# Kernel tuning notes

Hardware: AMD Instinct MI355X
Metric: run time of the kernel (lower is better)

Reference implementation:

```python
import jax, jax.numpy as jnp
import numpy as np


def setup_inputs() -> dict:
    key = jax.random.key(0)
    k1, k2, k3 = jax.random.split(key, 3)
    N, M, D = 8192, 32768, 64
    source_data = jax.random.normal(k1, (N, D), dtype=jnp.float32)
    target_data = jax.random.normal(k2, (M, D), dtype=jnp.float32)
    psi = jax.random.normal(k3, (M,), dtype=jnp.float32)
    return {"source_data": source_data, "target_data": target_data, "psi": psi}


def reference(source_data, target_data, psi):
    # cost[n, m] = ||x_n||^2 + ||y_m||^2 - 2 <x_n, y_m>
    sq_src = jnp.sum(source_data ** 2, axis=1, keepdims=True)          # [N, 1]
    sq_tgt = jnp.sum(target_data ** 2, axis=1)[None, :]                # [1, M]
    cost = sq_src + sq_tgt - 2.0 * jnp.einsum('nd,md->nm', source_data, target_data)
    out = jnp.min(cost - psi[None, :], axis=1) + jnp.mean(psi)         # [N]
    return out
```

## Files before the change

kernel.cpp:

```cpp
#include <hip/hip_runtime.h>
#include <stdint.h>

typedef float  f32x4v __attribute__((ext_vector_type(4)));
typedef short  s16x8  __attribute__((ext_vector_type(8)));

constexpr int D      = 64;
constexpr int SPLITS = 128;
constexpr int CHM    = 256;
constexpr int G      = 4;
constexpr int NT     = CHM / 16;

__device__ __forceinline__ unsigned short f2bf(float f) {
    unsigned int u = __float_as_uint(f);
    u = (u + 0x7FFFu + ((u >> 16) & 1u)) >> 16;
    return (unsigned short)u;
}

__device__ __forceinline__ void gload_lds16(const void* g, void* l) {
    __builtin_amdgcn_global_load_lds((__attribute__((address_space(1))) void*)g,
                                     (__attribute__((address_space(3))) void*)l, 16, 0, 0);
}
__device__ __forceinline__ void gload_lds4(const void* g, void* l) {
    __builtin_amdgcn_global_load_lds((__attribute__((address_space(1))) void*)g,
                                     (__attribute__((address_space(3))) void*)l, 4, 0, 0);
}

__global__ __launch_bounds__(256)
void prep(const float* __restrict__ X, const float* __restrict__ Y,
          const float* __restrict__ psi,
          unsigned short* __restrict__ Xb, unsigned short* __restrict__ Yb,
          float* __restrict__ t, float* __restrict__ sqx,
          float* __restrict__ psum_arr, int N, int M) {
    const int tid  = threadIdx.x;
    const int lane = tid & 63, wave = tid >> 6;
    const int r16  = lane & 15, q = lane >> 4;
    const int NYB = M >> 4, NXB = N >> 4;
    const int b = blockIdx.x;
    __shared__ float red[4];

    if (b < NYB) {
        const int row = b * 16 + wave * 4 + q;
        const float4 v = *reinterpret_cast<const float4*>(Y + (size_t)row * D + r16 * 4);
        uint2 p;
        p.x = (unsigned)f2bf(v.x) | ((unsigned)f2bf(v.y) << 16);
        p.y = (unsigned)f2bf(v.z) | ((unsigned)f2bf(v.w) << 16);
        *reinterpret_cast<uint2*>(Yb + (size_t)row * D + r16 * 4) = p;
        float s = v.x * v.x + v.y * v.y + v.z * v.z + v.w * v.w;
        #pragma unroll
        for (int off = 1; off <= 8; off <<= 1) s += __shfl_xor(s, off);
        if (r16 == 0) t[row] = s - psi[row];
    } else if (b < NYB + NXB) {
        const int row = (b - NYB) * 16 + wave * 4 + q;
        const float4 v = *reinterpret_cast<const float4*>(X + (size_t)row * D + r16 * 4);
        uint2 p;
        p.x = (unsigned)f2bf(-2.f * v.x) | ((unsigned)f2bf(-2.f * v.y) << 16);
        p.y = (unsigned)f2bf(-2.f * v.z) | ((unsigned)f2bf(-2.f * v.w) << 16);
        *reinterpret_cast<uint2*>(Xb + (size_t)row * D + r16 * 4) = p;
        float s = v.x * v.x + v.y * v.y + v.z * v.z + v.w * v.w;
        #pragma unroll
        for (int off = 1; off <= 8; off <<= 1) s += __shfl_xor(s, off);
        if (r16 == 0) sqx[row] = s;
    } else {
        const int g = b - NYB - NXB;
        float s = psi[g * 512 + tid] + psi[g * 512 + 256 + tid];
        #pragma unroll
        for (int off = 1; off <= 32; off <<= 1) s += __shfl_xor(s, off);
        if (lane == 0) red[wave] = s;
        __syncthreads();
        if (tid == 0) psum_arr[g] = red[0] + red[1] + red[2] + red[3];
    }
}

__global__ __launch_bounds__(256, 4)
void sdot_main(const unsigned short* __restrict__ Xb,
               const unsigned short* __restrict__ Yb,
               const float* __restrict__ t,
               float* __restrict__ partial, int M) {
    __shared__ __align__(16) unsigned short ly[CHM * D];
    __shared__ __align__(16) float lt[CHM];

    const int tid  = threadIdx.x;
    const int wave = tid >> 6, lane = tid & 63;
    const int quad = lane >> 4, r16 = lane & 15;
    const int chunk   = blockIdx.x;
    const int rowgrp  = blockIdx.y;
    const int m_begin = chunk * CHM;

    #pragma unroll
    for (int i = 0; i < 8; ++i) {
        const int idx = i * 256 + tid;
        const int row = idx >> 3, c = idx & 7;
        gload_lds16(Yb + (size_t)(m_begin + row) * D + ((c ^ (row & 7)) << 3),
                    &ly[(i * 256 + wave * 64) << 3]);
    }
    gload_lds4(t + m_begin + wave * 64 + lane, &lt[wave * 64]);

    s16x8 b[G][2];
    #pragma unroll
    for (int g = 0; g < G; ++g) {
        const int srow = rowgrp * 256 + wave * (G * 16) + g * 16 + r16;
        #pragma unroll
        for (int h = 0; h < 2; ++h)
            b[g][h] = *reinterpret_cast<const s16x8*>(Xb + (size_t)srow * D + h * 32 + quad * 8);
    }

    float rmin[G];
    #pragma unroll
    for (int g = 0; g < G; ++g) rmin[g] = 1e30f;

    asm volatile("s_waitcnt vmcnt(0)" ::: "memory");
    __builtin_amdgcn_s_barrier();

    const int csw0 = (quad ^ (r16 & 7)) << 3;
    const int csw1 = ((quad + 4) ^ (r16 & 7)) << 3;

#define SDOT_STEP(st, A_)                                                           \
    {                                                                               \
        const int trow = (st) * 16 + r16;                                           \
        const s16x8 a0 = *reinterpret_cast<const s16x8*>(&ly[trow * D + csw0]);     \
        const s16x8 a1 = *reinterpret_cast<const s16x8*>(&ly[trow * D + csw1]);     \
        const f32x4v tv4 = *reinterpret_cast<const f32x4v*>(&lt[(st) * 16 + quad * 4]); \
        __builtin_amdgcn_s_setprio(1);                                              \
        _Pragma("unroll")                                                           \
        for (int g = 0; g < G; ++g)                                                 \
            A_[g] = __builtin_amdgcn_mfma_f32_16x16x32_bf16(a0, b[g][0], tv4, 0, 0, 0); \
        _Pragma("unroll")                                                           \
        for (int g = 0; g < G; ++g)                                                 \
            A_[g] = __builtin_amdgcn_mfma_f32_16x16x32_bf16(a1, b[g][1], A_[g], 0, 0, 0); \
        __builtin_amdgcn_s_setprio(0);                                              \
    }
#define SDOT_FOLD(A_)                                                               \
    {                                                                               \
        _Pragma("unroll")                                                           \
        for (int g = 0; g < G; ++g)                                                 \
            rmin[g] = fminf(fminf(fminf(A_[g][0], A_[g][1]),                        \
                                  fminf(A_[g][2], A_[g][3])), rmin[g]);             \
    }

    f32x4v accA[G], accB[G];
    SDOT_STEP(0, accB);
    for (int p = 0; p < NT / 2 - 1; ++p) {
        SDOT_STEP(2 * p + 1, accA);  SDOT_FOLD(accB);
        SDOT_STEP(2 * p + 2, accB);  SDOT_FOLD(accA);
    }
    SDOT_STEP(NT - 1, accA);  SDOT_FOLD(accB);  SDOT_FOLD(accA);
#undef SDOT_STEP
#undef SDOT_FOLD

    #pragma unroll
    for (int off = 16; off <= 32; off <<= 1)
        #pragma unroll
        for (int g = 0; g < G; ++g)
            rmin[g] = fminf(rmin[g], __shfl_xor(rmin[g], off));

    if (quad == 0) {
        #pragma unroll
        for (int g = 0; g < G; ++g) {
            const int row = rowgrp * 256 + wave * (G * 16) + g * 16 + r16;
            partial[(size_t)row * SPLITS + chunk] = rmin[g];
        }
    }
}

__global__ __launch_bounds__(256)
void finalize(const float* __restrict__ sqx, const float* __restrict__ partial,
              const float* __restrict__ psum_arr, float* __restrict__ out, int M) {
    const int lane = threadIdx.x & 63, wave = threadIdx.x >> 6;
    const int row  = blockIdx.x * 4 + wave;
    float ps = psum_arr[lane];
    #pragma unroll
    for (int off = 1; off <= 32; off <<= 1) ps += __shfl_xor(ps, off);
    float pm = fminf(partial[(size_t)row * SPLITS + lane],
                     partial[(size_t)row * SPLITS + 64 + lane]);
    #pragma unroll
    for (int off = 1; off <= 32; off <<= 1) pm = fminf(pm, __shfl_xor(pm, off));
    if (lane == 0) out[row] = sqx[row] + ps / (float)M + pm;
}

extern "C" void kernel_launch(void* const* d_in, const int* in_sizes, int n_in,
                              void* d_out, int out_size, void* d_ws, size_t ws_size,
                              hipStream_t stream) {
    const float* X   = (const float*)d_in[0];
    const float* Y   = (const float*)d_in[1];
    const float* psi = (const float*)d_in[2];
    float* out = (float*)d_out;

    const int N = in_sizes[0] / D;
    const int M = in_sizes[2];

    char* ws = (char*)d_ws;
    unsigned short* Yb = (unsigned short*)ws;
    size_t off = (size_t)M * D * sizeof(unsigned short);
    unsigned short* Xb = (unsigned short*)(ws + off);
    off += (size_t)N * D * sizeof(unsigned short);
    float* t = (float*)(ws + off);
    off += (size_t)M * sizeof(float);
    float* sqx = (float*)(ws + off);
    off += (size_t)N * sizeof(float);
    float* partial = (float*)(ws + off);
    off += (size_t)N * SPLITS * sizeof(float);
    float* psum_arr = (float*)(ws + off);

    prep<<<(M >> 4) + (N >> 4) + 64, 256, 0, stream>>>(X, Y, psi, Xb, Yb, t, sqx, psum_arr, N, M);
    sdot_main<<<dim3(SPLITS, N / 256), 256, 0, stream>>>(Xb, Yb, t, partial, M);
    finalize<<<N / 4, 256, 0, stream>>>(sqx, partial, psum_arr, out, M);
}
```

Measured before the change: 103.9 us.

## Loop over double-buffered Y tiles per block with fewer M splits

```diff
diff --git a/kernel.cpp b/kernel.cpp
--- a/kernel.cpp
+++ b/kernel.cpp
@@ -5,10 +5,9 @@
 typedef short  s16x8  __attribute__((ext_vector_type(8)));
 
 constexpr int D      = 64;
-constexpr int SPLITS = 128;
-constexpr int CHM    = 256;
+constexpr int SPLITS = 32;
+constexpr int TILE_M = 128;
 constexpr int G      = 4;
-constexpr int NT     = CHM / 16;
 
 __device__ __forceinline__ unsigned short f2bf(float f) {
     unsigned int u = __float_as_uint(f);
@@ -76,24 +75,17 @@
                const unsigned short* __restrict__ Yb,
                const float* __restrict__ t,
                float* __restrict__ partial, int M) {
-    __shared__ __align__(16) unsigned short ly[CHM * D];
-    __shared__ __align__(16) float lt[CHM];
+    __shared__ __align__(16) unsigned short ly[2][TILE_M * 64];
+    __shared__ __align__(16) float lt[2][256];
 
     const int tid  = threadIdx.x;
     const int wave = tid >> 6, lane = tid & 63;
     const int quad = lane >> 4, r16 = lane & 15;
-    const int chunk   = blockIdx.x;
-    const int rowgrp  = blockIdx.y;
-    const int m_begin = chunk * CHM;
-
-    #pragma unroll
-    for (int i = 0; i < 8; ++i) {
-        const int idx = i * 256 + tid;
-        const int row = idx >> 3, c = idx & 7;
-        gload_lds16(Yb + (size_t)(m_begin + row) * D + ((c ^ (row & 7)) << 3),
-                    &ly[(i * 256 + wave * 64) << 3]);
-    }
-    gload_lds4(t + m_begin + wave * 64 + lane, &lt[wave * 64]);
+    const int chunk  = blockIdx.x;
+    const int rowgrp = blockIdx.y;
+    const int CH      = M / SPLITS;
+    const int m_begin = chunk * CH;
+    const int NTT     = CH / TILE_M;
 
     s16x8 b[G][2];
     #pragma unroll
@@ -108,6 +100,18 @@
     #pragma unroll
     for (int g = 0; g < G; ++g) rmin[g] = 1e30f;
 
+    auto stage = [&](int buf, int mb) {
+        #pragma unroll
+        for (int i = 0; i < 4; ++i) {
+            const int idx = i * 256 + tid;
+            const int row = idx >> 3, c = idx & 7;
+            gload_lds16(Yb + (size_t)(mb + row) * D + ((c ^ (row & 7)) << 3),
+                        &ly[buf][(i * 256 + wave * 64) << 3]);
+        }
+        gload_lds4(t + mb + wave * 64 + lane, &lt[buf][wave * 64]);
+    };
+
+    stage(0, m_begin);
     asm volatile("s_waitcnt vmcnt(0)" ::: "memory");
     __builtin_amdgcn_s_barrier();
 
@@ -117,9 +121,9 @@
 #define SDOT_STEP(st, A_)                                                           \
     {                                                                               \
         const int trow = (st) * 16 + r16;                                           \
-        const s16x8 a0 = *reinterpret_cast<const s16x8*>(&ly[trow * D + csw0]);     \
-        const s16x8 a1 = *reinterpret_cast<const s16x8*>(&ly[trow * D + csw1]);     \
-        const f32x4v tv4 = *reinterpret_cast<const f32x4v*>(&lt[(st) * 16 + quad * 4]); \
+        const s16x8 a0 = *reinterpret_cast<const s16x8*>(&ly[buf][trow * 64 + csw0]); \
+        const s16x8 a1 = *reinterpret_cast<const s16x8*>(&ly[buf][trow * 64 + csw1]); \
+        const f32x4v tv4 = *reinterpret_cast<const f32x4v*>(&lt[buf][(st) * 16 + quad * 4]); \
         __builtin_amdgcn_s_setprio(1);                                              \
         _Pragma("unroll")                                                           \
         for (int g = 0; g < G; ++g)                                                 \
@@ -138,12 +142,21 @@
     }
 
     f32x4v accA[G], accB[G];
-    SDOT_STEP(0, accB);
-    for (int p = 0; p < NT / 2 - 1; ++p) {
-        SDOT_STEP(2 * p + 1, accA);  SDOT_FOLD(accB);
-        SDOT_STEP(2 * p + 2, accB);  SDOT_FOLD(accA);
-    }
-    SDOT_STEP(NT - 1, accA);  SDOT_FOLD(accB);  SDOT_FOLD(accA);
+    for (int tI = 0; tI < NTT; ++tI) {
+        const int buf = tI & 1;
+        if (tI + 1 < NTT) stage(buf ^ 1, m_begin + (tI + 1) * TILE_M);
+
+        SDOT_STEP(0, accB);
+        #pragma unroll
+        for (int p = 0; p < 3; ++p) {
+            SDOT_STEP(2 * p + 1, accA);  SDOT_FOLD(accB);
+            SDOT_STEP(2 * p + 2, accB);  SDOT_FOLD(accA);
+        }
+        SDOT_STEP(7, accA);  SDOT_FOLD(accB);  SDOT_FOLD(accA);
+
+        asm volatile("s_waitcnt vmcnt(0)" ::: "memory");
+        __builtin_amdgcn_s_barrier();
+    }
 #undef SDOT_STEP
 #undef SDOT_FOLD
 
@@ -170,8 +183,7 @@
     float ps = psum_arr[lane];
     #pragma unroll
     for (int off = 1; off <= 32; off <<= 1) ps += __shfl_xor(ps, off);
-    float pm = fminf(partial[(size_t)row * SPLITS + lane],
-                     partial[(size_t)row * SPLITS + 64 + lane]);
+    float pm = (lane < SPLITS) ? partial[(size_t)row * SPLITS + lane] : 1e30f;
     #pragma unroll
     for (int off = 1; off <= 32; off <<= 1) pm = fminf(pm, __shfl_xor(pm, off));
     if (lane == 0) out[row] = sqx[row] + ps / (float)M + pm;
```

Result: no change. 103.1 us (-0.8%).
